# Performance work log

Hardware: AMD Instinct MI355X
Metric: run time of the kernel (lower is better)

Reference implementation:

```python
import jax, jax.numpy as jnp
import numpy as np

LATENT = 512
VOCAB = 32000
START_TOKEN = 0
END_TOKEN = 1
BATCH = 128
BN_EPS = 1e-5


def setup_inputs() -> dict:
    key = jax.random.key(0)
    k = jax.random.split(key, 10)
    s = 0.02
    L, V = LATENT, VOCAB
    return {
        "z": jax.random.normal(k[0], (BATCH, L), dtype=jnp.float32),
        "emb": jax.random.normal(k[1], (V, L), dtype=jnp.float32) * s,      # embedding table
        "Wp1": jax.random.normal(k[2], (2 * L, L), dtype=jnp.float32) * s,  # project layer 1
        "bp1": jnp.zeros((2 * L,), jnp.float32),
        "Wp2": jax.random.normal(k[3], (2 * L, 2 * L), dtype=jnp.float32) * s,  # project layer 2
        "bp2": jnp.zeros((2 * L,), jnp.float32),
        "Wih": jax.random.normal(k[4], (4 * L, L), dtype=jnp.float32) * s,  # LSTMCell input weights (i,f,g,o)
        "Whh": jax.random.normal(k[5], (4 * L, L), dtype=jnp.float32) * s,
        "bih": jnp.zeros((4 * L,), jnp.float32),
        "bhh": jnp.zeros((4 * L,), jnp.float32),
        "Wo1": jax.random.normal(k[6], (2 * L, L), dtype=jnp.float32) * s,  # output MLP layer 1
        "bo1": jnp.zeros((2 * L,), jnp.float32),
        "bn_g": jnp.ones((2 * L,), jnp.float32),   # BatchNorm1d (eval mode)
        "bn_b": jnp.zeros((2 * L,), jnp.float32),
        "bn_m": jnp.zeros((2 * L,), jnp.float32),
        "bn_v": jnp.ones((2 * L,), jnp.float32),
        "Wo2": jax.random.normal(k[7], (V - 1, 2 * L), dtype=jnp.float32) * s,  # vocab head
        "bo2": jnp.zeros((V - 1,), jnp.float32),
        "max_len": 50,
    }


def _elu01(x):
    # nn.ELU(alpha=0.1)
    return jnp.where(x > 0, x, 0.1 * (jnp.exp(x) - 1.0))


def _run(z, emb, Wp1, bp1, Wp2, bp2, Wih, Whh, bih, bhh,
         Wo1, bo1, bn_g, bn_b, bn_m, bn_v, Wo2, bo2, max_len):
    B, L = z.shape
    # project z -> (h, c); dropout inactive in eval mode
    h1 = jax.nn.relu(z @ Wp1.T + bp1)
    hc = _elu01(h1 @ Wp2.T + bp2)
    h, c = jnp.split(hc, 2, axis=1)            # each [B, L]
    e0 = jnp.broadcast_to(emb[START_TOKEN], (B, L))
    keys = jax.random.split(jax.random.key(42), max_len)
    inv_std = bn_g / jnp.sqrt(bn_v + BN_EPS)   # fused BN scale (eval)

    def step(carry, key):
        h, c, e = carry
        gates = e @ Wih.T + bih + h @ Whh.T + bhh
        i, f, g, o = jnp.split(gates, 4, axis=1)  # torch LSTMCell gate order
        c = jax.nn.sigmoid(f) * c + jax.nn.sigmoid(i) * jnp.tanh(g)
        h = jax.nn.sigmoid(o) * jnp.tanh(c)
        a = jax.nn.relu(h) @ Wo1.T + bo1
        a = (a - bn_m) * inv_std + bn_b
        logits = jax.nn.relu(a) @ Wo2.T + bo2      # [B, V-1]
        logp = jax.nn.log_softmax(logits, axis=-1)
        # Categorical sampling via Gumbel-max
        sample = jnp.argmax(logits + jax.random.gumbel(key, logits.shape), axis=-1)
        lp = jnp.take_along_axis(logp, sample[:, None], axis=1)[:, 0]
        ent = -jnp.sum(jnp.exp(logp) * logp, axis=-1)
        return (h, c, jnp.take(emb, sample, axis=0)), (sample, lp, ent)

    _, (xs, lps, ents) = jax.lax.scan(step, (h, c, e0), keys)
    x = xs.T          # [B, T]
    lps = lps.T       # [B, T]
    ents = ents.T     # [B, T]
    # first END occurrence (argmax returns first max; replicates torch semantics incl. its length-1 quirk)
    end_pos = jnp.argmax((x == END_TOKEN).astype(jnp.float32), axis=1)
    seq_len = end_pos + 1
    seq_len = jnp.where(seq_len == 1, max_len, seq_len)
    mask = jnp.arange(max_len)[None, :] < seq_len[:, None]
    x_out = jnp.where(mask, x + 1, 0)                      # pad_sequence(padding=-1) then +1 -> 0 pad
    lp_out = jnp.where(mask, lps, 0.0)                     # padded per-step log-probs
    ent_mean = jnp.sum(jnp.where(mask, ents, 0.0), axis=1) / seq_len.astype(ents.dtype)
    return x_out, lp_out, ent_mean


def reference(z, emb, Wp1, bp1, Wp2, bp2, Wih, Whh, bih, bhh,
              Wo1, bo1, bn_g, bn_b, bn_m, bn_v, Wo2, bo2, max_len):
    return _run(z, emb, Wp1, bp1, Wp2, bp2, Wih, Whh, bih, bhh,
                Wo1, bo1, bn_g, bn_b, bn_m, bn_v, Wo2, bo2, max_len)
```

## Files before the change

### kernel.cpp

```cpp
#include <hip/hip_runtime.h>
#include <stdint.h>
#include <math.h>

#define BATCH  128
#define NV     31999
#define NSTEP  50
#define NPB    500
#define TINYF  1.17549435e-38f

typedef __attribute__((ext_vector_type(8))) short bf16x8;
typedef __attribute__((ext_vector_type(4))) float f32x4;
typedef __attribute__((ext_vector_type(4))) unsigned int u32x4;

__host__ __device__ __forceinline__ void tf2x32(uint32_t k0, uint32_t k1,
                                                uint32_t x0, uint32_t x1,
                                                uint32_t& o0, uint32_t& o1) {
  uint32_t k2 = k0 ^ k1 ^ 0x1BD11BDAu;
  x0 += k0; x1 += k1;
#define TF_R(r) { x0 += x1; x1 = (x1 << (r)) | (x1 >> (32 - (r))); x1 ^= x0; }
  TF_R(13) TF_R(15) TF_R(26) TF_R(6)
  x0 += k1; x1 += k2 + 1u;
  TF_R(17) TF_R(29) TF_R(16) TF_R(24)
  x0 += k2; x1 += k0 + 2u;
  TF_R(13) TF_R(15) TF_R(26) TF_R(6)
  x0 += k0; x1 += k1 + 3u;
  TF_R(17) TF_R(29) TF_R(16) TF_R(24)
  x0 += k1; x1 += k2 + 4u;
  TF_R(13) TF_R(15) TF_R(26) TF_R(6)
  x0 += k2; x1 += k0 + 5u;
#undef TF_R
  o0 = x0; o1 = x1;
}

__device__ __forceinline__ float sigm(float x) { return 1.0f / (1.0f + expf(-x)); }

__device__ __forceinline__ float gumbelv(uint32_t k0, uint32_t k1, uint32_t f) {
  uint32_t o0, o1; tf2x32(k0, k1, 0u, f, o0, o1);
  uint32_t bits = o0 ^ o1;
  float ff = __uint_as_float((bits >> 9) | 0x3f800000u) - 1.0f;
  float u = ff + TINYF;
  return -logf(-logf(u));
}

__device__ __forceinline__ unsigned short bfhi(float x) {
  uint32_t u = __float_as_uint(x);
  u += 0x7fffu + ((u >> 16) & 1u);
  return (unsigned short)(u >> 16);
}
__device__ __forceinline__ void split2(float x, unsigned short& h, unsigned short& l) {
  unsigned short hh = bfhi(x);
  float hf = __uint_as_float(((uint32_t)hh) << 16);
  h = hh; l = bfhi(x - hf);
}

#define MFMA3(ah, al, bh, bl, c)                                            \
  c = __builtin_amdgcn_mfma_f32_16x16x32_bf16(ah, bh, c, 0, 0, 0);          \
  c = __builtin_amdgcn_mfma_f32_16x16x32_bf16(ah, bl, c, 0, 0, 0);          \
  c = __builtin_amdgcn_mfma_f32_16x16x32_bf16(al, bh, c, 0, 0, 0);

__global__ __launch_bounds__(256) void gemm_part(
    const float* __restrict__ A, int lda,
    const float* __restrict__ Wa, const float* __restrict__ Wb,
    int ks, int K, int N, int KC, float* __restrict__ part)
{
  __shared__ float As[32][132];
  __shared__ float Ws[32][68];
  const int tx = threadIdx.x;
  const int n0 = blockIdx.x * 64;
  const int kc = blockIdx.y;
  const int cg = tx & 15, rg = tx >> 4;
  float acc[8][4] = {};
  const int kend = (kc + 1) * KC;
  for (int kk = kc * KC; kk < kend; kk += 32) {
    __syncthreads();
#pragma unroll
    for (int i = 0; i < 16; ++i) {
      int e = tx + 256 * i; int b = e >> 5, k = e & 31;
      As[k][b] = A[b * lda + kk + k];
    }
#pragma unroll
    for (int i = 0; i < 8; ++i) {
      int e = tx + 256 * i; int n = e >> 5, k = e & 31;
      int nn = n0 + n, kg = kk + k;
      float w;
      if (kg < ks) w = Wa[(size_t)nn * ks + kg];
      else         w = Wb[(size_t)nn * (K - ks) + (kg - ks)];
      Ws[k][n] = w;
    }
    __syncthreads();
#pragma unroll
    for (int k = 0; k < 32; ++k) {
      float4 a0 = *(const float4*)&As[k][rg * 8];
      float4 a1 = *(const float4*)&As[k][rg * 8 + 4];
      float4 wv = *(const float4*)&Ws[k][cg * 4];
      float ar[8] = {a0.x, a0.y, a0.z, a0.w, a1.x, a1.y, a1.z, a1.w};
      float wr[4] = {wv.x, wv.y, wv.z, wv.w};
#pragma unroll
      for (int r = 0; r < 8; ++r)
#pragma unroll
        for (int c = 0; c < 4; ++c) acc[r][c] += ar[r] * wr[c];
    }
  }
  size_t base = (size_t)kc * BATCH * N;
#pragma unroll
  for (int r = 0; r < 8; ++r) {
    int row = rg * 8 + r;
    float4 v4 = make_float4(acc[r][0], acc[r][1], acc[r][2], acc[r][3]);
    *(float4*)&part[base + (size_t)row * N + n0 + cg * 4] = v4;
  }
}

__global__ void k_reduce_relu(const float* __restrict__ part, int nkc,
                              const float* __restrict__ bias,
                              float* __restrict__ out, int N) {
  int i = blockIdx.x * 256 + threadIdx.x;
  int n = i % N;
  float s = bias[n];
  for (int kc = 0; kc < nkc; ++kc) s += part[(size_t)kc * BATCH * N + i];
  out[i] = fmaxf(s, 0.0f);
}

__global__ void k_reduce_elu_split(const float* __restrict__ part, int nkc,
                                   const float* __restrict__ bias,
                                   unsigned short* __restrict__ xh,
                                   unsigned short* __restrict__ xl,
                                   float* __restrict__ cbuf) {
  int i = blockIdx.x * 256 + threadIdx.x;
  int b = i >> 10, n = i & 1023;
  float s = bias[n];
  for (int kc = 0; kc < nkc; ++kc) s += part[(size_t)kc * BATCH * 1024 + i];
  float e = (s > 0.0f) ? s : 0.1f * (expf(s) - 1.0f);
  if (n < 512) {
    unsigned short h_, l_; split2(e, h_, l_);
    xh[b * 1024 + 512 + n] = h_; xl[b * 1024 + 512 + n] = l_;
  } else cbuf[b * 512 + (n - 512)] = e;
}

__global__ void k_fill_e0(const float* __restrict__ emb,
                          unsigned short* __restrict__ xh,
                          unsigned short* __restrict__ xl) {
  int i = blockIdx.x * 256 + threadIdx.x;
  int b = i >> 9, k = i & 511;
  unsigned short h_, l_; split2(emb[k], h_, l_);
  xh[b * 1024 + k] = h_; xl[b * 1024 + k] = l_;
}

__global__ void k_prep_gates(const float* __restrict__ Wih, const float* __restrict__ Whh,
                             const float* __restrict__ bih, const float* __restrict__ bhh,
                             unsigned short* __restrict__ Wh, unsigned short* __restrict__ Wl,
                             float* __restrict__ bg) {
  int i = blockIdx.x * 256 + threadIdx.x;
  int idx8 = i * 8;
  int n = idx8 >> 10, k0 = idx8 & 1023;
  const float* src = (k0 < 512) ? (Wih + (size_t)n * 512 + k0)
                                : (Whh + (size_t)n * 512 + (k0 - 512));
  float4 a = *(const float4*)src, b = *(const float4*)(src + 4);
  float wv[8] = {a.x, a.y, a.z, a.w, b.x, b.y, b.z, b.w};
  unsigned short hh[8], ll[8];
#pragma unroll
  for (int q = 0; q < 8; ++q) split2(wv[q], hh[q], ll[q]);
  u32x4 h4, l4;
#pragma unroll
  for (int q = 0; q < 4; ++q) {
    h4[q] = (uint32_t)hh[2 * q] | ((uint32_t)hh[2 * q + 1] << 16);
    l4[q] = (uint32_t)ll[2 * q] | ((uint32_t)ll[2 * q + 1] << 16);
  }
  *(u32x4*)(Wh + (size_t)idx8) = h4;
  *(u32x4*)(Wl + (size_t)idx8) = l4;
  if (i < 256) {
#pragma unroll
    for (int q = 0; q < 8; ++q) bg[i * 8 + q] = bih[i * 8 + q] + bhh[i * 8 + q];
  }
}

__global__ void k_prep_out1(const float* __restrict__ Wo1, const float* __restrict__ bo1,
                            const float* __restrict__ g, const float* __restrict__ bb,
                            const float* __restrict__ m, const float* __restrict__ v,
                            unsigned short* __restrict__ Wh, unsigned short* __restrict__ Wl,
                            float* __restrict__ S, float* __restrict__ T) {
  int i = blockIdx.x * 256 + threadIdx.x;
  int idx8 = i * 8;
  float4 a = *(const float4*)(Wo1 + idx8), b = *(const float4*)(Wo1 + idx8 + 4);
  float wv[8] = {a.x, a.y, a.z, a.w, b.x, b.y, b.z, b.w};
  unsigned short hh[8], ll[8];
#pragma unroll
  for (int q = 0; q < 8; ++q) split2(wv[q], hh[q], ll[q]);
  u32x4 h4, l4;
#pragma unroll
  for (int q = 0; q < 4; ++q) {
    h4[q] = (uint32_t)hh[2 * q] | ((uint32_t)hh[2 * q + 1] << 16);
    l4[q] = (uint32_t)ll[2 * q] | ((uint32_t)ll[2 * q + 1] << 16);
  }
  *(u32x4*)(Wh + (size_t)idx8) = h4;
  *(u32x4*)(Wl + (size_t)idx8) = l4;
  if (i < 128) {
#pragma unroll
    for (int q = 0; q < 8; ++q) {
      int n = i * 8 + q;
      float s = g[n] / sqrtf(v[n] + 1e-5f);
      S[n] = s;
      T[n] = (bo1[n] - m[n]) * s + bb[n];
    }
  }
}

__global__ void k_prep_wo2(const float* __restrict__ W,
                           unsigned short* __restrict__ Wh, unsigned short* __restrict__ Wl,
                           int total8) {
  int i = blockIdx.x * 256 + threadIdx.x;
  if (i >= total8) return;
  const float* wp = W + (size_t)i * 8;
  float4 a = *(const float4*)wp, b = *(const float4*)(wp + 4);
  float wv[8] = {a.x, a.y, a.z, a.w, b.x, b.y, b.z, b.w};
  unsigned short hh[8], ll[8];
#pragma unroll
  for (int q = 0; q < 8; ++q) split2(wv[q], hh[q], ll[q]);
  u32x4 h4, l4;
#pragma unroll
  for (int q = 0; q < 4; ++q) {
    h4[q] = (uint32_t)hh[2 * q] | ((uint32_t)hh[2 * q + 1] << 16);
    l4[q] = (uint32_t)ll[2 * q] | ((uint32_t)ll[2 * q + 1] << 16);
  }
  *(u32x4*)(Wh + (size_t)i * 8) = h4;
  *(u32x4*)(Wl + (size_t)i * 8) = l4;
}

__global__ __launch_bounds__(256) void k_gates(
    const unsigned short* __restrict__ Ah, const unsigned short* __restrict__ Al,
    const unsigned short* __restrict__ Wh, const unsigned short* __restrict__ Wl,
    const float* __restrict__ bg, float* __restrict__ cbuf,
    unsigned short* __restrict__ xh, unsigned short* __restrict__ xl,
    unsigned short* __restrict__ rhh, unsigned short* __restrict__ rhl)
{
  __shared__ __align__(16) unsigned char SM[40960];
  unsigned short (*WHb)[2][64][40] = (unsigned short(*)[2][64][40])SM;
  unsigned short (*WLb)[2][64][40] = (unsigned short(*)[2][64][40])(SM + 20480);
  const int tx = threadIdx.x;
  const int lane = tx & 63, w = tx >> 6;
  const int l15 = lane & 15, g4 = lane >> 4;
  const int gblk = blockIdx.x;
  const int arow0 = w * 32 + l15, ak = g4 * 8;
  const int sr = tx >> 2, sq = tx & 3;
  const int grow = (sr >> 4) * 512 + gblk * 16 + (sr & 15);
  const size_t wbase = (size_t)grow * 1024;

  f32x4 acc[2][4] = {};
  u32x4 RH[2][2], RL[2][2];
  bf16x8 QH[2][2][2], QL[2][2][2];

  auto ldW = [&](int set, int t) {
    const int kk = t * 64 + sq * 16;
    RH[set][0] = *(const u32x4*)(Wh + wbase + kk);
    RH[set][1] = *(const u32x4*)(Wh + wbase + kk + 8);
    RL[set][0] = *(const u32x4*)(Wl + wbase + kk);
    RL[set][1] = *(const u32x4*)(Wl + wbase + kk + 8);
  };
  auto stW = [&](int set, int buf) {
    const int kc = sq >> 1, ko = (sq & 1) * 16;
    *(u32x4*)&WHb[buf][kc][sr][ko]     = RH[set][0];
    *(u32x4*)&WHb[buf][kc][sr][ko + 8] = RH[set][1];
    *(u32x4*)&WLb[buf][kc][sr][ko]     = RL[set][0];
    *(u32x4*)&WLb[buf][kc][sr][ko + 8] = RL[set][1];
  };
  auto ldA = [&](int set, int t) {
#pragma unroll
    for (int rf = 0; rf < 2; ++rf)
#pragma unroll
      for (int kc = 0; kc < 2; ++kc) {
        size_t ao = (size_t)(arow0 + rf * 16) * 1024 + t * 64 + kc * 32 + ak;
        QH[set][rf][kc] = *(const bf16x8*)(Ah + ao);
        QL[set][rf][kc] = *(const bf16x8*)(Al + ao);
      }
  };
  auto comp = [&](int buf, int set) {
#pragma unroll
    for (int kc = 0; kc < 2; ++kc)
#pragma unroll
      for (int cf = 0; cf < 4; ++cf) {
        int col = cf * 16 + l15;
        bf16x8 bh = *(const bf16x8*)&WHb[buf][kc][col][ak];
        bf16x8 bl = *(const bf16x8*)&WLb[buf][kc][col][ak];
#pragma unroll
        for (int rf = 0; rf < 2; ++rf) { MFMA3(QH[set][rf][kc], QL[set][rf][kc], bh, bl, acc[rf][cf]); }
      }
  };

  ldW(0, 0); ldW(1, 1); ldA(0, 0);
  stW(0, 0); __syncthreads();
  for (int t = 0; t < 16; ++t) {
    const int pb = t & 1;
    if (t < 14) ldW(pb, t + 2);
    if (t < 15) ldA(pb ^ 1, t + 1);
    comp(pb, pb);
    if (t < 15) stW(pb ^ 1, pb ^ 1);
    __syncthreads();
  }
  float* gex = (float*)SM;
#pragma unroll
  for (int rf = 0; rf < 2; ++rf)
#pragma unroll
    for (int cf = 0; cf < 4; ++cf)
#pragma unroll
      for (int r = 0; r < 4; ++r) {
        int brow = w * 32 + rf * 16 + g4 * 4 + r;
        gex[(cf * 128 + brow) * 17 + l15] = acc[rf][cf][r];
      }
  __syncthreads();
#pragma unroll
  for (int i = 0; i < 8; ++i) {
    int e = tx + 256 * i;
    int b = e >> 4, lj = e & 15;
    int jg = gblk * 16 + lj;
    float gi = gex[(0 * 128 + b) * 17 + lj] + bg[jg];
    float gf = gex[(1 * 128 + b) * 17 + lj] + bg[512 + jg];
    float gg = gex[(2 * 128 + b) * 17 + lj] + bg[1024 + jg];
    float go = gex[(3 * 128 + b) * 17 + lj] + bg[1536 + jg];
    float co = cbuf[b * 512 + jg];
    float cn = sigm(gf) * co + sigm(gi) * tanhf(gg);
    float hn = sigm(go) * tanhf(cn);
    cbuf[b * 512 + jg] = cn;
    unsigned short h_, l_;
    split2(hn, h_, l_);
    xh[b * 1024 + 512 + jg] = h_; xl[b * 1024 + 512 + jg] = l_;
    float r = fmaxf(hn, 0.0f);
    split2(r, h_, l_);
    rhh[b * 512 + jg] = h_; rhl[b * 512 + jg] = l_;
  }
}

__global__ __launch_bounds__(256) void k_out1(
    const unsigned short* __restrict__ Ah, const unsigned short* __restrict__ Al,
    const unsigned short* __restrict__ Wh, const unsigned short* __restrict__ Wl,
    const float* __restrict__ S, const float* __restrict__ T,
    unsigned short* __restrict__ r2h, unsigned short* __restrict__ r2l)
{
  __shared__ __align__(16) unsigned char SM[40960];
  unsigned short (*WHb)[2][64][40] = (unsigned short(*)[2][64][40])SM;
  unsigned short (*WLb)[2][64][40] = (unsigned short(*)[2][64][40])(SM + 20480);
  const int tx = threadIdx.x;
  const int lane = tx & 63, w = tx >> 6;
  const int l15 = lane & 15, g4 = lane >> 4;
  const int n0 = blockIdx.x * 64;
  const int arow0 = w * 32 + l15, ak = g4 * 8;
  const int sr = tx >> 2, sq = tx & 3;
  const size_t wbase = (size_t)(n0 + sr) * 512;

  f32x4 acc[2][4] = {};
  u32x4 RH[2][2], RL[2][2];
  bf16x8 QH[2][2][2], QL[2][2][2];

  auto ldW = [&](int set, int t) {
    const int kk = t * 64 + sq * 16;
    RH[set][0] = *(const u32x4*)(Wh + wbase + kk);
    RH[set][1] = *(const u32x4*)(Wh + wbase + kk + 8);
    RL[set][0] = *(const u32x4*)(Wl + wbase + kk);
    RL[set][1] = *(const u32x4*)(Wl + wbase + kk + 8);
  };
  auto stW = [&](int set, int buf) {
    const int kc = sq >> 1, ko = (sq & 1) * 16;
    *(u32x4*)&WHb[buf][kc][sr][ko]     = RH[set][0];
    *(u32x4*)&WHb[buf][kc][sr][ko + 8] = RH[set][1];
    *(u32x4*)&WLb[buf][kc][sr][ko]     = RL[set][0];
    *(u32x4*)&WLb[buf][kc][sr][ko + 8] = RL[set][1];
  };
  auto ldA = [&](int set, int t) {
#pragma unroll
    for (int rf = 0; rf < 2; ++rf)
#pragma unroll
      for (int kc = 0; kc < 2; ++kc) {
        size_t ao = (size_t)(arow0 + rf * 16) * 512 + t * 64 + kc * 32 + ak;
        QH[set][rf][kc] = *(const bf16x8*)(Ah + ao);
        QL[set][rf][kc] = *(const bf16x8*)(Al + ao);
      }
  };
  auto comp = [&](int buf, int set) {
#pragma unroll
    for (int kc = 0; kc < 2; ++kc)
#pragma unroll
      for (int cf = 0; cf < 4; ++cf) {
        int col = cf * 16 + l15;
        bf16x8 bh = *(const bf16x8*)&WHb[buf][kc][col][ak];
        bf16x8 bl = *(const bf16x8*)&WLb[buf][kc][col][ak];
#pragma unroll
        for (int rf = 0; rf < 2; ++rf) { MFMA3(QH[set][rf][kc], QL[set][rf][kc], bh, bl, acc[rf][cf]); }
      }
  };

  ldW(0, 0); ldW(1, 1); ldA(0, 0);
  stW(0, 0); __syncthreads();
  for (int t = 0; t < 8; ++t) {
    const int pb = t & 1;
    if (t < 6) ldW(pb, t + 2);
    if (t < 7) ldA(pb ^ 1, t + 1);
    comp(pb, pb);
    if (t < 7) stW(pb ^ 1, pb ^ 1);
    __syncthreads();
  }
#pragma unroll
  for (int cf = 0; cf < 4; ++cf) {
    int n = n0 + cf * 16 + l15;
    float s = S[n], t = T[n];
#pragma unroll
    for (int rf = 0; rf < 2; ++rf)
#pragma unroll
      for (int r = 0; r < 4; ++r) {
        int row = w * 32 + rf * 16 + g4 * 4 + r;
        float v = fmaxf(acc[rf][cf][r] * s + t, 0.0f);
        unsigned short h_, l_; split2(v, h_, l_);
        r2h[row * 1024 + n] = h_; r2l[row * 1024 + n] = l_;
      }
  }
}

template<int PRE>
__global__ __launch_bounds__(512, 4) void k_vocab(
    const unsigned short* __restrict__ Ah, const unsigned short* __restrict__ Al,
    const unsigned short* __restrict__ Wh, const unsigned short* __restrict__ Wl,
    const float* __restrict__ Wf, const float* __restrict__ bias,
    uint32_t key0, uint32_t key1,
    float* __restrict__ vpmax, float* __restrict__ vps1, float* __restrict__ vps2,
    float* __restrict__ vpbv, float* __restrict__ vpbl, int* __restrict__ vpbi)
{
  __shared__ __align__(16) unsigned char SM[40960];
  unsigned short (*WHb)[2][64][40] = (unsigned short(*)[2][64][40])SM;
  unsigned short (*WLb)[2][64][40] = (unsigned short(*)[2][64][40])(SM + 20480);
  const int tx = threadIdx.x;
  const int lane = tx & 63, w = tx >> 6;
  const int l15 = lane & 15, g4 = lane >> 4;
  const int n0 = blockIdx.x * 64;
  const int arow = w * 16 + l15, ak = g4 * 8;
  const int sr = tx >> 3, sq = tx & 7;
  int grow = n0 + sr; if (grow >= NV) grow = NV - 1;
  const size_t wbase = (size_t)grow * 1024;
  const int skc = sq >> 2, sko = (sq & 3) * 8;

  f32x4 acc[4] = {};
  u32x4 RH[3], RL[3];
  float4 RF[3][2];
  bf16x8 QH[2][2], QL[2][2];
  float gv[16];

  auto ldW = [&](int s, int t) {
    const int kk = t * 64 + sq * 8;
    if (PRE) {
      RH[s] = *(const u32x4*)(Wh + wbase + kk);
      RL[s] = *(const u32x4*)(Wl + wbase + kk);
    } else {
      RF[s][0] = *(const float4*)(Wf + wbase + kk);
      RF[s][1] = *(const float4*)(Wf + wbase + kk + 4);
    }
  };
  auto stW = [&](int s, int buf) {
    if (PRE) {
      *(u32x4*)&WHb[buf][skc][sr][sko] = RH[s];
      *(u32x4*)&WLb[buf][skc][sr][sko] = RL[s];
    } else {
      float fv[8] = {RF[s][0].x, RF[s][0].y, RF[s][0].z, RF[s][0].w,
                     RF[s][1].x, RF[s][1].y, RF[s][1].z, RF[s][1].w};
      unsigned short hh[8], ll[8];
#pragma unroll
      for (int q = 0; q < 8; ++q) split2(fv[q], hh[q], ll[q]);
#pragma unroll
      for (int q = 0; q < 8; ++q) { WHb[buf][skc][sr][sko + q] = hh[q]; WLb[buf][skc][sr][sko + q] = ll[q]; }
    }
  };
  auto ldA = [&](int s, int t) {
#pragma unroll
    for (int kc = 0; kc < 2; ++kc) {
      size_t ao = (size_t)arow * 1024 + t * 64 + kc * 32 + ak;
      QH[s][kc] = *(const bf16x8*)(Ah + ao);
      QL[s][kc] = *(const bf16x8*)(Al + ao);
    }
  };
  auto comp = [&](int buf, int s) {
#pragma unroll
    for (int kc = 0; kc < 2; ++kc)
#pragma unroll
      for (int cf = 0; cf < 4; ++cf) {
        int col = cf * 16 + l15;
        bf16x8 bh = *(const bf16x8*)&WHb[buf][kc][col][ak];
        bf16x8 bl = *(const bf16x8*)&WLb[buf][kc][col][ak];
        MFMA3(QH[s][kc], QL[s][kc], bh, bl, acc[cf]);
      }
  };

  ldW(0, 0); ldW(1, 1); ldW(2, 2); ldA(0, 0);
  stW(0, 0); __syncthreads();
#pragma unroll
  for (int t = 0; t < 16; ++t) {
    const int pb = t & 1;
    if (t < 13) ldW(t % 3, t + 3);
    if (t < 15) ldA((t + 1) & 1, t + 1);
    {
      int row_t = w * 16 + g4 * 4 + (t >> 2);
      int v_t = n0 + (t & 3) * 16 + l15;
      if (v_t >= NV) v_t = 0;
      gv[t] = gumbelv(key0, key1, (uint32_t)row_t * 31999u + (uint32_t)v_t);
    }
    comp(pb, t & 1);
    if (t < 15) stW((t + 1) % 3, pb ^ 1);
    __syncthreads();
  }
  float bias_c[4]; int vcol[4];
#pragma unroll
  for (int cf = 0; cf < 4; ++cf) {
    int v = n0 + cf * 16 + l15;
    vcol[cf] = v;
    bias_c[cf] = (v < NV) ? bias[v] : 0.0f;
  }
#pragma unroll
  for (int reg = 0; reg < 4; ++reg) {
    int row = w * 16 + g4 * 4 + reg;
    float lv[4], pv[4];
    float mm = -INFINITY;
#pragma unroll
    for (int cf = 0; cf < 4; ++cf) {
      if (vcol[cf] < NV) {
        float l = acc[cf][reg] + bias_c[cf];
        lv[cf] = l; pv[cf] = l + gv[reg * 4 + cf];
        mm = fmaxf(mm, l);
      } else { lv[cf] = -INFINITY; pv[cf] = -INFINITY; }
    }
    for (int d = 1; d <= 8; d <<= 1) mm = fmaxf(mm, __shfl_xor(mm, d));
    float s1 = 0.0f, s2 = 0.0f;
#pragma unroll
    for (int cf = 0; cf < 4; ++cf)
      if (vcol[cf] < NV) { float t = lv[cf] - mm; float e = expf(t); s1 += e; s2 += e * t; }
    for (int d = 1; d <= 8; d <<= 1) { s1 += __shfl_xor(s1, d); s2 += __shfl_xor(s2, d); }
    float bv = -INFINITY, bl_ = 0.0f; int bi = 0x7fffffff;
#pragma unroll
    for (int cf = 0; cf < 4; ++cf)
      if (pv[cf] > bv || (pv[cf] == bv && vcol[cf] < bi)) { bv = pv[cf]; bi = vcol[cf]; bl_ = lv[cf]; }
    for (int d = 1; d <= 8; d <<= 1) {
      float ov = __shfl_xor(bv, d); int oi = __shfl_xor(bi, d); float ol = __shfl_xor(bl_, d);
      if (ov > bv || (ov == bv && oi < bi)) { bv = ov; bi = oi; bl_ = ol; }
    }
    if (l15 == 0) {
      int o = row * NPB + blockIdx.x;
      vpmax[o] = mm; vps1[o] = s1; vps2[o] = s2;
      vpbv[o] = bv; vpbl[o] = bl_; vpbi[o] = bi;
    }
  }
}

__global__ __launch_bounds__(256) void k_final_sample(
    const float* __restrict__ vpmax, const float* __restrict__ vps1,
    const float* __restrict__ vps2, const float* __restrict__ vpbv,
    const float* __restrict__ vpbl, const int* __restrict__ vpbi,
    int t, int* __restrict__ xhist, float* __restrict__ lph,
    float* __restrict__ enth, const float* __restrict__ emb,
    unsigned short* __restrict__ xh, unsigned short* __restrict__ xl) {
  int b = blockIdx.x, tid = threadIdx.x;
  int lane = tid & 63, wv = tid >> 6;
  __shared__ float sM[4], sS1[4], sS2[4], sBV[4], sBL[4];
  __shared__ int sBI[4];
  float M = -INFINITY;
  for (int p = tid; p < NPB; p += 256) M = fmaxf(M, vpmax[b * NPB + p]);
  for (int d = 32; d; d >>= 1) M = fmaxf(M, __shfl_xor(M, d));
  if (lane == 0) sM[wv] = M;
  __syncthreads();
  M = fmaxf(fmaxf(sM[0], sM[1]), fmaxf(sM[2], sM[3]));
  float S1 = 0.0f, S2 = 0.0f, bv = -INFINITY, bl = 0.0f; int bi = 0x7fffffff;
  for (int p = tid; p < NPB; p += 256) {
    int o = b * NPB + p;
    float dm = vpmax[o] - M;
    float sc = expf(dm);
    S1 += vps1[o] * sc;
    S2 += (vps2[o] + dm * vps1[o]) * sc;
    float v = vpbv[o]; int ii = vpbi[o];
    if (v > bv || (v == bv && ii < bi)) { bv = v; bi = ii; bl = vpbl[o]; }
  }
  for (int d = 32; d; d >>= 1) {
    S1 += __shfl_xor(S1, d); S2 += __shfl_xor(S2, d);
    float ov = __shfl_xor(bv, d); int oi = __shfl_xor(bi, d); float ol = __shfl_xor(bl, d);
    if (ov > bv || (ov == bv && oi < bi)) { bv = ov; bi = oi; bl = ol; }
  }
  if (lane == 0) { sS1[wv] = S1; sS2[wv] = S2; sBV[wv] = bv; sBL[wv] = bl; sBI[wv] = bi; }
  __syncthreads();
  S1 = sS1[0] + sS1[1] + sS1[2] + sS1[3];
  S2 = sS2[0] + sS2[1] + sS2[2] + sS2[3];
  bv = -INFINITY; bi = 0x7fffffff; bl = 0.0f;
#pragma unroll
  for (int q = 0; q < 4; ++q) {
    if (sBV[q] > bv || (sBV[q] == bv && sBI[q] < bi)) { bv = sBV[q]; bi = sBI[q]; bl = sBL[q]; }
  }
  float logZ = logf(S1);
  if (tid == 0) {
    xhist[t * 128 + b] = bi;
    lph[t * 128 + b] = bl - M - logZ;
    enth[t * 128 + b] = logZ - S2 / S1;
  }
  const float* er = emb + (size_t)bi * 512;
  for (int k = tid; k < 512; k += 256) {
    unsigned short h_, l_; split2(er[k], h_, l_);
    xh[b * 1024 + k] = h_; xl[b * 1024 + k] = l_;
  }
}

__global__ void k_finalize(const int* __restrict__ xhist, const float* __restrict__ lph,
                           const float* __restrict__ enth, float* __restrict__ out) {
  int b = blockIdx.x, lane = threadIdx.x;
  int tok = -1, cand = 1 << 20;
  if (lane < NSTEP) {
    tok = xhist[lane * 128 + b];
    if (tok == 1) cand = lane;
  }
  int e = cand;
  for (int d = 32; d; d >>= 1) e = min(e, __shfl_xor(e, d));
  int end_pos = (e >= (1 << 20)) ? 0 : e;
  int seq_len = end_pos + 1;
  if (seq_len == 1) seq_len = NSTEP;
  float ent = 0.0f;
  if (lane < NSTEP) {
    bool msk = lane < seq_len;
    out[b * NSTEP + lane]        = msk ? (float)(tok + 1) : 0.0f;
    out[6400 + b * NSTEP + lane] = msk ? lph[lane * 128 + b] : 0.0f;
    ent = msk ? enth[lane * 128 + b] : 0.0f;
  }
  for (int d = 32; d; d >>= 1) ent += __shfl_xor(ent, d);
  if (lane == 0) out[12800 + b] = ent / (float)seq_len;
}

extern "C" void kernel_launch(void* const* d_in, const int* in_sizes, int n_in,
                              void* d_out, int out_size, void* d_ws, size_t ws_size,
                              hipStream_t stream) {
  const float* z    = (const float*)d_in[0];
  const float* emb  = (const float*)d_in[1];
  const float* Wp1  = (const float*)d_in[2];
  const float* bp1  = (const float*)d_in[3];
  const float* Wp2  = (const float*)d_in[4];
  const float* bp2  = (const float*)d_in[5];
  const float* Wih  = (const float*)d_in[6];
  const float* Whh  = (const float*)d_in[7];
  const float* bih  = (const float*)d_in[8];
  const float* bhh  = (const float*)d_in[9];
  const float* Wo1  = (const float*)d_in[10];
  const float* bo1  = (const float*)d_in[11];
  const float* bng  = (const float*)d_in[12];
  const float* bnb  = (const float*)d_in[13];
  const float* bnm  = (const float*)d_in[14];
  const float* bnv  = (const float*)d_in[15];
  const float* Wo2  = (const float*)d_in[16];
  const float* bo2  = (const float*)d_in[17];
  float* out = (float*)d_out;
  (void)in_sizes; (void)n_in; (void)out_size;

  char* base = (char*)d_ws;
  size_t off = 0;
  auto alloc = [&](size_t bytes) -> void* {
    void* p = base + off;
    off = (off + bytes + 255) & ~(size_t)255;
    return p;
  };
  unsigned short* xh[2]; unsigned short* xl[2];
  xh[0] = (unsigned short*)alloc(128 * 1024 * 2);
  xl[0] = (unsigned short*)alloc(128 * 1024 * 2);
  xh[1] = (unsigned short*)alloc(128 * 1024 * 2);
  xl[1] = (unsigned short*)alloc(128 * 1024 * 2);
  float* cbuf = (float*)alloc(128 * 512 * 4);
  unsigned short* rhh = (unsigned short*)alloc(128 * 512 * 2);
  unsigned short* rhl = (unsigned short*)alloc(128 * 512 * 2);
  unsigned short* r2h = (unsigned short*)alloc(128 * 1024 * 2);
  unsigned short* r2l = (unsigned short*)alloc(128 * 1024 * 2);
  float* h1    = (float*)alloc(128 * 1024 * 4);
  float* apart = (float*)alloc((size_t)8 * 128 * 1024 * 4);
  unsigned short* Wgh = (unsigned short*)alloc((size_t)2048 * 1024 * 2);
  unsigned short* Wgl = (unsigned short*)alloc((size_t)2048 * 1024 * 2);
  float* bg = (float*)alloc(2048 * 4);
  unsigned short* Wo1h = (unsigned short*)alloc((size_t)1024 * 512 * 2);
  unsigned short* Wo1l = (unsigned short*)alloc((size_t)1024 * 512 * 2);
  float* Sbn = (float*)alloc(1024 * 4);
  float* Tbn = (float*)alloc(1024 * 4);
  float* vpmax = (float*)alloc((size_t)NPB * 128 * 4);
  float* vps1  = (float*)alloc((size_t)NPB * 128 * 4);
  float* vps2  = (float*)alloc((size_t)NPB * 128 * 4);
  float* vpbv  = (float*)alloc((size_t)NPB * 128 * 4);
  float* vpbl  = (float*)alloc((size_t)NPB * 128 * 4);
  int*   vpbi  = (int*)alloc((size_t)NPB * 128 * 4);
  int*   xhist = (int*)alloc(50 * 128 * 4);
  float* lph   = (float*)alloc(50 * 128 * 4);
  float* enth  = (float*)alloc(50 * 128 * 4);
  size_t wo2_elems = (size_t)NV * 1024;
  bool pre = ws_size >= off + 2 * wo2_elems * 2 + (1 << 20);
  unsigned short* Wo2h = nullptr; unsigned short* Wo2l = nullptr;
  if (pre) {
    Wo2h = (unsigned short*)alloc(wo2_elems * 2);
    Wo2l = (unsigned short*)alloc(wo2_elems * 2);
  }

  uint32_t outk[100];
  for (int t = 0; t < 50; ++t) {
    uint32_t y0, y1;
    tf2x32(0u, 42u, 0u, (uint32_t)t, y0, y1);
    outk[2 * t] = y0; outk[2 * t + 1] = y1;
  }

  k_prep_gates<<<1024, 256, 0, stream>>>(Wih, Whh, bih, bhh, Wgh, Wgl, bg);
  k_prep_out1<<<256, 256, 0, stream>>>(Wo1, bo1, bng, bnb, bnm, bnv, Wo1h, Wo1l, Sbn, Tbn);
  if (pre) {
    int total8 = (int)(wo2_elems / 8);
    k_prep_wo2<<<(total8 + 255) / 256, 256, 0, stream>>>(Wo2, Wo2h, Wo2l, total8);
  }

  k_fill_e0<<<256, 256, 0, stream>>>(emb, xh[0], xl[0]);
  gemm_part<<<dim3(16, 4), 256, 0, stream>>>(z, 512, Wp1, Wp1, 512, 512, 1024, 128, apart);
  k_reduce_relu<<<512, 256, 0, stream>>>(apart, 4, bp1, h1, 1024);
  gemm_part<<<dim3(16, 8), 256, 0, stream>>>(h1, 1024, Wp2, Wp2, 1024, 1024, 1024, 128, apart);
  k_reduce_elu_split<<<512, 256, 0, stream>>>(apart, 8, bp2, xh[0], xl[0], cbuf);

  for (int t = 0; t < NSTEP; ++t) {
    int ri = t & 1, wi = ri ^ 1;
    k_gates<<<32, 256, 0, stream>>>(xh[ri], xl[ri], Wgh, Wgl, bg, cbuf,
                                    xh[wi], xl[wi], rhh, rhl);
    k_out1<<<16, 256, 0, stream>>>(rhh, rhl, Wo1h, Wo1l, Sbn, Tbn, r2h, r2l);
    if (pre)
      k_vocab<1><<<NPB, 512, 0, stream>>>(r2h, r2l, Wo2h, Wo2l, Wo2, bo2,
                                          outk[2 * t], outk[2 * t + 1],
                                          vpmax, vps1, vps2, vpbv, vpbl, vpbi);
    else
      k_vocab<0><<<NPB, 512, 0, stream>>>(r2h, r2l, nullptr, nullptr, Wo2, bo2,
                                          outk[2 * t], outk[2 * t + 1],
                                          vpmax, vps1, vps2, vpbv, vpbl, vpbi);
    k_final_sample<<<128, 256, 0, stream>>>(vpmax, vps1, vps2, vpbv, vpbl, vpbi,
                                            t, xhist, lph, enth, emb, xh[wi], xl[wi]);
  }
  k_finalize<<<128, 64, 0, stream>>>(xhist, lph, enth, out);
}
```

Baseline: 4.445 ms.

## Use four-stage LDS ring in vocab GEMM to halve barriers per k-step

Result: faster. 4.275 ms, median of 2 (-3.8%).

```diff
diff --git a/kernel.cpp b/kernel.cpp
--- a/kernel.cpp
+++ b/kernel.cpp
@@ -421,9 +421,9 @@
     float* __restrict__ vpmax, float* __restrict__ vps1, float* __restrict__ vps2,
     float* __restrict__ vpbv, float* __restrict__ vpbl, int* __restrict__ vpbi)
 {
-  __shared__ __align__(16) unsigned char SM[40960];
+  __shared__ __align__(16) unsigned char SM[81920];
   unsigned short (*WHb)[2][64][40] = (unsigned short(*)[2][64][40])SM;
-  unsigned short (*WLb)[2][64][40] = (unsigned short(*)[2][64][40])(SM + 20480);
+  unsigned short (*WLb)[2][64][40] = (unsigned short(*)[2][64][40])(SM + 40960);
   const int tx = threadIdx.x;
   const int lane = tx & 63, w = tx >> 6;
   const int l15 = lane & 15, g4 = lane >> 4;
@@ -435,10 +435,10 @@
   const int skc = sq >> 2, sko = (sq & 3) * 8;
 
   f32x4 acc[4] = {};
-  u32x4 RH[3], RL[3];
-  float4 RF[3][2];
+  u32x4 RH[4], RL[4];
+  float4 RF[4][2];
   bf16x8 QH[2][2], QL[2][2];
-  float gv[16];
+  float gvv[16];
 
   auto ldW = [&](int s, int t) {
     const int kk = t * 64 + sq * 8;
@@ -483,22 +483,28 @@
         MFMA3(QH[s][kc], QL[s][kc], bh, bl, acc[cf]);
       }
   };
-
-  ldW(0, 0); ldW(1, 1); ldW(2, 2); ldA(0, 0);
-  stW(0, 0); __syncthreads();
-#pragma unroll
-  for (int t = 0; t < 16; ++t) {
-    const int pb = t & 1;
-    if (t < 13) ldW(t % 3, t + 3);
-    if (t < 15) ldA((t + 1) & 1, t + 1);
-    {
-      int row_t = w * 16 + g4 * 4 + (t >> 2);
-      int v_t = n0 + (t & 3) * 16 + l15;
-      if (v_t >= NV) v_t = 0;
-      gv[t] = gumbelv(key0, key1, (uint32_t)row_t * 31999u + (uint32_t)v_t);
-    }
-    comp(pb, t & 1);
-    if (t < 15) stW((t + 1) % 3, pb ^ 1);
+  auto gum = [&](int t) {
+    int row_t = w * 16 + g4 * 4 + (t >> 2);
+    int v_t = n0 + (t & 3) * 16 + l15;
+    if (v_t >= NV) v_t = 0;
+    gvv[t] = gumbelv(key0, key1, (uint32_t)row_t * 31999u + (uint32_t)v_t);
+  };
+
+  ldW(0, 0); ldW(1, 1); ldW(2, 2); ldW(3, 3); ldA(0, 0);
+  stW(0, 0); stW(1, 1);
+  __syncthreads();
+#pragma unroll
+  for (int tp = 0; tp < 16; tp += 2) {
+    if (tp + 4 < 16) ldW((tp + 4) & 3, tp + 4);
+    if (tp + 1 < 16) ldA((tp + 1) & 1, tp + 1);
+    gum(tp);
+    comp(tp & 3, tp & 1);
+    if (tp + 2 < 16) stW((tp + 2) & 3, (tp + 2) & 3);
+    if (tp + 5 < 16) ldW((tp + 5) & 3, tp + 5);
+    if (tp + 2 < 16) ldA((tp + 2) & 1, tp + 2);
+    gum(tp + 1);
+    comp((tp + 1) & 3, (tp + 1) & 1);
+    if (tp + 3 < 16) stW((tp + 3) & 3, (tp + 3) & 3);
     __syncthreads();
   }
   float bias_c[4]; int vcol[4];
@@ -517,7 +523,7 @@
     for (int cf = 0; cf < 4; ++cf) {
       if (vcol[cf] < NV) {
         float l = acc[cf][reg] + bias_c[cf];
-        lv[cf] = l; pv[cf] = l + gv[reg * 4 + cf];
+        lv[cf] = l; pv[cf] = l + gvv[reg * 4 + cf];
         mm = fmaxf(mm, l);
       } else { lv[cf] = -INFINITY; pv[cf] = -INFINITY; }
     }
```
